# Kernel tuning notes

Measured on AMD Instinct MI355X. Metric: run time of the kernel, lower is better.

## Reference

```python
import jax, jax.numpy as jnp
import numpy as np

TEMP = 1.0

def setup_inputs() -> dict:
    key = jax.random.key(0)
    k1, k2, k3 = jax.random.split(key, 3)
    B, C, H, W = 8, 256, 64, 64
    h = jax.random.normal(k1, (B, C, H, W), dtype=jnp.float32)
    xs = jax.random.normal(k2, (B, C, H, W), dtype=jnp.float32)
    ys = jax.random.normal(k3, (B, C, H, W), dtype=jnp.float32)
    return {"h": h, "xs": xs, "ys": ys}

def reference(h, xs, ys):
    B, C, H, W = h.shape
    Bs, Cs, Hs, Ws = xs.shape
    hf = h.reshape(B, C, H * W)            # [B, C, N]   N = H*W
    xf = xs.reshape(Bs, Cs, Hs * Ws)       # [B, C, M]   M = Hs*Ws
    yf = ys.reshape(ys.shape[0], ys.shape[1], -1)  # [B, C, M]
    # attention[b, n, m] = sum_c h[b,c,n] * xs[b,c,m]
    attn = jnp.einsum('bcn,bcm->bnm', hf, xf)
    attn = jax.nn.softmax(attn / TEMP, axis=2)  # softmax over support positions m
    # xxs[b, c, n] = sum_m ys[b,c,m] * attn[b,n,m]
    xxs = jnp.einsum('bcm,bnm->bcn', yf, attn)
    return xxs.reshape(B, C, H, W)
```

## Files before the change

kernel.cpp:

```cpp
#include <hip/hip_runtime.h>
#include <stdint.h>

#define B_ 8
#define C_ 256
#define N_ 4096
#define M_ 4096
#define NT 64
#define MT 64
#define PP 72
#define L2E 1.44269504f

typedef _Float16 f16x8 __attribute__((ext_vector_type(8)));
typedef _Float16 f16x4 __attribute__((ext_vector_type(4)));
typedef float f32x4 __attribute__((ext_vector_type(4)));

__device__ __forceinline__ void async16(const _Float16* g, _Float16* l) {
    __builtin_amdgcn_global_load_lds(
        (const __attribute__((address_space(1))) void*)g,
        (__attribute__((address_space(3))) void*)l, 16, 0, 0);
}

__global__ __launch_bounds__(256) void kPre(const float* __restrict__ xs,
                                            const float* __restrict__ ys,
                                            _Float16* __restrict__ kt,
                                            _Float16* __restrict__ vb) {
    int bx = blockIdx.x;
    int t = threadIdx.x;
    if (bx < 2048) {
        __shared__ float tile[64][65];
        int b = bx >> 8, rem = bx & 255;
        int c0 = (rem >> 6) * 64, m0 = (rem & 63) * 64;
        int cl = t >> 4, m4 = (t & 15) * 4;
#pragma unroll
        for (int i = 0; i < 4; i++) {
            int c = c0 + cl + i * 16;
            const float4 v = *(const float4*)(xs + ((size_t)(b * C_ + c) * M_) + m0 + m4);
            tile[m4 + 0][cl + i * 16] = v.x;
            tile[m4 + 1][cl + i * 16] = v.y;
            tile[m4 + 2][cl + i * 16] = v.z;
            tile[m4 + 3][cl + i * 16] = v.w;
        }
        __syncthreads();
        int ml = t >> 4, c4 = (t & 15) * 4;
#pragma unroll
        for (int i = 0; i < 4; i++) {
            int m = m0 + ml + i * 16;
            f16x4 o;
            o[0] = (_Float16)tile[ml + i * 16][c4 + 0];
            o[1] = (_Float16)tile[ml + i * 16][c4 + 1];
            o[2] = (_Float16)tile[ml + i * 16][c4 + 2];
            o[3] = (_Float16)tile[ml + i * 16][c4 + 3];
            *(f16x4*)(kt + ((size_t)(b * M_ + m) * C_) + c0 + c4) = o;
        }
    } else {
        size_t i = ((size_t)(bx - 2048) * 256 + t) * 4;
        float4 v = *(const float4*)(ys + i);
        f16x4 o;
        o[0] = (_Float16)v.x; o[1] = (_Float16)v.y;
        o[2] = (_Float16)v.z; o[3] = (_Float16)v.w;
        *(f16x4*)(vb + i) = o;
    }
}

__global__ __launch_bounds__(256, 2) void kAttn(const float* __restrict__ h,
                                                const _Float16* __restrict__ kt,
                                                const _Float16* __restrict__ vb,
                                                float* __restrict__ out) {
    __shared__ _Float16 sK[2][MT * 256];
    __shared__ _Float16 sP[NT * PP];
    __shared__ float sAlpha[NT];
    __shared__ float sL[NT];
    __shared__ int sFlag[2];

    const int t = threadIdx.x;
    const int w = t >> 6, lane = t & 63, quad = lane >> 4, l15 = lane & 15;
    const int b = blockIdx.x >> 6;
    const int n0 = (blockIdx.x & 63) * NT;
    const int nb = w * 16;
    const int cb = w * 64;

    const _Float16* srcKb = kt + (size_t)b * M_ * C_;
    const _Float16* srcVb = vb + (size_t)b * C_ * M_;

    if (t == 0) { sFlag[0] = 0; sFlag[1] = 0; }

    {
        int cl = t >> 4, n4 = (t & 15) * 4;
        for (int i = 0; i < 16; i++) {
            int c = i * 16 + cl;
            const float4 v = *(const float4*)(h + ((size_t)(b * C_ + c) * N_) + n0 + n4);
            float xv[4] = {v.x, v.y, v.z, v.w};
#pragma unroll
            for (int j = 0; j < 4; j++) {
                int row = n4 + j;
                sK[1][row * 256 + (((c >> 3) ^ (row & 31)) << 3) + (c & 7)] = (_Float16)xv[j];
            }
        }
#pragma unroll
        for (int j = 0; j < 8; j++) {
            int row = w * 16 + j * 2 + (lane >> 5);
            int logi = (lane & 31) ^ (row & 31);
            async16(srcKb + (size_t)row * C_ + logi * 8, &sK[0][(w * 16 + j * 2) * 256]);
        }
    }
    __syncthreads();

    f16x8 qf[8];
    {
        int qrow = nb + l15;
#pragma unroll
        for (int ks = 0; ks < 8; ks++)
            qf[ks] = *(const f16x8*)(&sK[1][qrow * 256 + ((((ks << 2) + quad) ^ (qrow & 31)) << 3)]);
    }

    f32x4 o[4][4];
#pragma unroll
    for (int i = 0; i < 4; i++)
#pragma unroll
        for (int j = 0; j < 4; j++)
            o[i][j] = (f32x4){0.f, 0.f, 0.f, 0.f};

    float mst[4], lp[4];
#pragma unroll
    for (int r = 0; r < 4; r++) { mst[r] = -3.0e38f; lp[r] = 0.f; }

    for (int it = 0; it < M_ / MT; it++) {
        const int cur = it & 1, nxt = cur ^ 1;
        const int m0i = it * MT;
        __syncthreads();

        if (t == 0) sFlag[nxt] = 0;

        if (it + 1 < M_ / MT) {
            const _Float16* srcK = srcKb + (size_t)(m0i + MT) * C_;
#pragma unroll
            for (int j = 0; j < 8; j++) {
                int row = w * 16 + j * 2 + (lane >> 5);
                int logi = (lane & 31) ^ (row & 31);
                async16(srcK + (size_t)row * C_ + logi * 8, &sK[nxt][(w * 16 + j * 2) * 256]);
            }
        }

        f16x8 vf[2][4];
#pragma unroll
        for (int ks = 0; ks < 2; ks++)
#pragma unroll
            for (int ct = 0; ct < 4; ct++) {
                int vrow = cb + ct * 16 + l15;
                vf[ks][ct] = *(const f16x8*)(srcVb + (size_t)vrow * M_ + m0i + ks * 32 + quad * 8);
            }

        f32x4 s[4];
#pragma unroll
        for (int mt = 0; mt < 4; mt++) s[mt] = (f32x4){0.f, 0.f, 0.f, 0.f};
#pragma unroll
        for (int ks = 0; ks < 8; ks++) {
#pragma unroll
            for (int mt = 0; mt < 4; mt++) {
                int krow = mt * 16 + l15;
                f16x8 bk = *(const f16x8*)(&sK[cur][krow * 256 + ((((ks << 2) + quad) ^ (krow & 31)) << 3)]);
                s[mt] = __builtin_amdgcn_mfma_f32_16x16x32_f16(qf[ks], bk, s[mt], 0, 0, 0);
            }
        }

#pragma unroll
        for (int r = 0; r < 4; r++) {
            float rowmax = fmaxf(fmaxf(s[0][r], s[1][r]), fmaxf(s[2][r], s[3][r]));
#pragma unroll
            for (int off = 1; off < 16; off <<= 1)
                rowmax = fmaxf(rowmax, __shfl_xor(rowmax, off, 64));
            float al = 1.0f;
            if (rowmax > mst[r]) {
                al = exp2f((mst[r] - rowmax) * L2E);
                mst[r] = rowmax;
            }
            float psum = 0.f;
#pragma unroll
            for (int mt = 0; mt < 4; mt++) {
                float p = exp2f((s[mt][r] - mst[r]) * L2E);
                s[mt][r] = p;
                psum += p;
            }
            lp[r] = lp[r] * al + psum;
            int row = nb + quad * 4 + r;
            if (l15 == 0) {
                sAlpha[row] = al;
                if (al != 1.0f) atomicOr(&sFlag[cur], 1);
            }
#pragma unroll
            for (int mt = 0; mt < 4; mt++)
                sP[row * PP + mt * 16 + l15] = (_Float16)s[mt][r];
        }
        __syncthreads();

        if (sFlag[cur]) {
            float av[4];
#pragma unroll
            for (int nt = 0; nt < 4; nt++) av[nt] = sAlpha[nt * 16 + l15];
#pragma unroll
            for (int ct = 0; ct < 4; ct++)
#pragma unroll
                for (int nt = 0; nt < 4; nt++) {
                    o[ct][nt][0] *= av[nt];
                    o[ct][nt][1] *= av[nt];
                    o[ct][nt][2] *= av[nt];
                    o[ct][nt][3] *= av[nt];
                }
        }

#pragma unroll
        for (int ks = 0; ks < 2; ks++) {
#pragma unroll
            for (int nt = 0; nt < 4; nt++) {
                f16x8 bp = *(const f16x8*)(sP + (nt * 16 + l15) * PP + ks * 32 + quad * 8);
#pragma unroll
                for (int ct = 0; ct < 4; ct++)
                    o[ct][nt] = __builtin_amdgcn_mfma_f32_16x16x32_f16(vf[ks][ct], bp, o[ct][nt], 0, 0, 0);
            }
        }
    }

#pragma unroll
    for (int r = 0; r < 4; r++) {
#pragma unroll
        for (int off = 1; off < 16; off <<= 1)
            lp[r] += __shfl_xor(lp[r], off, 64);
        if (l15 == 0) sL[nb + quad * 4 + r] = lp[r];
    }
    __syncthreads();
    float linv[4];
#pragma unroll
    for (int nt = 0; nt < 4; nt++) linv[nt] = 1.0f / sL[nt * 16 + l15];
#pragma unroll
    for (int ct = 0; ct < 4; ct++)
#pragma unroll
        for (int nt = 0; nt < 4; nt++)
#pragma unroll
            for (int r = 0; r < 4; r++) {
                int c = cb + ct * 16 + quad * 4 + r;
                out[((size_t)(b * C_ + c)) * N_ + n0 + nt * 16 + l15] = o[ct][nt][r] * linv[nt];
            }
}

extern "C" void kernel_launch(void* const* d_in, const int* in_sizes, int n_in,
                              void* d_out, int out_size, void* d_ws, size_t ws_size,
                              hipStream_t stream) {
    const float* h  = (const float*)d_in[0];
    const float* xs = (const float*)d_in[1];
    const float* ys = (const float*)d_in[2];
    float* out = (float*)d_out;

    _Float16* kt  = (_Float16*)d_ws;
    _Float16* vbb = kt + (size_t)B_ * M_ * C_;

    kPre<<<dim3(2048 + 8192), 256, 0, stream>>>(xs, ys, kt, vbb);
    kAttn<<<dim3(B_ * (N_ / NT)), 256, 0, stream>>>(h, kt, vbb, out);
}
```

Baseline: 359.6 us.

## Transpose QK MFMA, simplify softmax reductions, replace syncthreads with tuned waitcnt barriers

Swaps the MFMA operand order for S so each lane holds one query row's scores. Row max and sum then need only two cross-quad shuffles instead of four per row, and P can be stored as packed f16x4 writes. Full __syncthreads are replaced by explicit s_waitcnt plus s_barrier, and V global loads are hoisted ahead of the K async prefetch behind a sched_barrier. The MFMA sections are wrapped in s_setprio to favour matrix issue. The manual waitcnt placement risks stalls or races if the counter semantics for global_load_lds are misjudged, for example vmcnt(0) at the loop top also waits on the V loads.

```diff
diff --git a/kernel.cpp b/kernel.cpp
--- a/kernel.cpp
+++ b/kernel.cpp
@@ -103,7 +103,8 @@
             async16(srcKb + (size_t)row * C_ + logi * 8, &sK[0][(w * 16 + j * 2) * 256]);
         }
     }
-    __syncthreads();
+    asm volatile("s_waitcnt lgkmcnt(0)" ::: "memory");
+    __builtin_amdgcn_s_barrier();
 
     f16x8 qf[8];
     {
@@ -112,6 +113,7 @@
         for (int ks = 0; ks < 8; ks++)
             qf[ks] = *(const f16x8*)(&sK[1][qrow * 256 + ((((ks << 2) + quad) ^ (qrow & 31)) << 3)]);
     }
+    asm volatile("s_waitcnt lgkmcnt(0)" ::: "memory");
 
     f32x4 o[4][4];
 #pragma unroll
@@ -120,16 +122,25 @@
         for (int j = 0; j < 4; j++)
             o[i][j] = (f32x4){0.f, 0.f, 0.f, 0.f};
 
-    float mst[4], lp[4];
-#pragma unroll
-    for (int r = 0; r < 4; r++) { mst[r] = -3.0e38f; lp[r] = 0.f; }
+    float mst = -3.0e38f, lp = 0.f;
 
     for (int it = 0; it < M_ / MT; it++) {
         const int cur = it & 1, nxt = cur ^ 1;
         const int m0i = it * MT;
-        __syncthreads();
+        asm volatile("s_waitcnt vmcnt(0)" ::: "memory");
+        __builtin_amdgcn_s_barrier();
 
         if (t == 0) sFlag[nxt] = 0;
+
+        f16x8 vf[2][4];
+#pragma unroll
+        for (int ks = 0; ks < 2; ks++)
+#pragma unroll
+            for (int ct = 0; ct < 4; ct++) {
+                int vrow = cb + ct * 16 + l15;
+                vf[ks][ct] = *(const f16x8*)(srcVb + (size_t)vrow * M_ + m0i + ks * 32 + quad * 8);
+            }
+        __builtin_amdgcn_sched_barrier(0);
 
         if (it + 1 < M_ / MT) {
             const _Float16* srcK = srcKb + (size_t)(m0i + MT) * C_;
@@ -141,57 +152,59 @@
             }
         }
 
-        f16x8 vf[2][4];
-#pragma unroll
-        for (int ks = 0; ks < 2; ks++)
-#pragma unroll
-            for (int ct = 0; ct < 4; ct++) {
-                int vrow = cb + ct * 16 + l15;
-                vf[ks][ct] = *(const f16x8*)(srcVb + (size_t)vrow * M_ + m0i + ks * 32 + quad * 8);
-            }
-
         f32x4 s[4];
 #pragma unroll
         for (int mt = 0; mt < 4; mt++) s[mt] = (f32x4){0.f, 0.f, 0.f, 0.f};
+        __builtin_amdgcn_s_setprio(1);
 #pragma unroll
         for (int ks = 0; ks < 8; ks++) {
 #pragma unroll
             for (int mt = 0; mt < 4; mt++) {
                 int krow = mt * 16 + l15;
                 f16x8 bk = *(const f16x8*)(&sK[cur][krow * 256 + ((((ks << 2) + quad) ^ (krow & 31)) << 3)]);
-                s[mt] = __builtin_amdgcn_mfma_f32_16x16x32_f16(qf[ks], bk, s[mt], 0, 0, 0);
-            }
-        }
-
-#pragma unroll
-        for (int r = 0; r < 4; r++) {
-            float rowmax = fmaxf(fmaxf(s[0][r], s[1][r]), fmaxf(s[2][r], s[3][r]));
-#pragma unroll
-            for (int off = 1; off < 16; off <<= 1)
-                rowmax = fmaxf(rowmax, __shfl_xor(rowmax, off, 64));
-            float al = 1.0f;
-            if (rowmax > mst[r]) {
-                al = exp2f((mst[r] - rowmax) * L2E);
-                mst[r] = rowmax;
-            }
-            float psum = 0.f;
-#pragma unroll
-            for (int mt = 0; mt < 4; mt++) {
-                float p = exp2f((s[mt][r] - mst[r]) * L2E);
+                s[mt] = __builtin_amdgcn_mfma_f32_16x16x32_f16(bk, qf[ks], s[mt], 0, 0, 0);
+            }
+        }
+        __builtin_amdgcn_s_setprio(0);
+
+        float rowmax = fmaxf(fmaxf(fmaxf(s[0][0], s[0][1]), fmaxf(s[0][2], s[0][3])),
+                             fmaxf(fmaxf(s[1][0], s[1][1]), fmaxf(s[1][2], s[1][3])));
+        rowmax = fmaxf(rowmax, fmaxf(fmaxf(fmaxf(s[2][0], s[2][1]), fmaxf(s[2][2], s[2][3])),
+                                     fmaxf(fmaxf(s[3][0], s[3][1]), fmaxf(s[3][2], s[3][3]))));
+        rowmax = fmaxf(rowmax, __shfl_xor(rowmax, 16, 64));
+        rowmax = fmaxf(rowmax, __shfl_xor(rowmax, 32, 64));
+        float al = 1.0f;
+        if (rowmax > mst) {
+            al = exp2f((mst - rowmax) * L2E);
+            mst = rowmax;
+        }
+        const float mb = mst * L2E;
+        float psum = 0.f;
+#pragma unroll
+        for (int mt = 0; mt < 4; mt++)
+#pragma unroll
+            for (int r = 0; r < 4; r++) {
+                float p = exp2f(s[mt][r] * L2E - mb);
                 s[mt][r] = p;
                 psum += p;
             }
-            lp[r] = lp[r] * al + psum;
-            int row = nb + quad * 4 + r;
-            if (l15 == 0) {
-                sAlpha[row] = al;
-                if (al != 1.0f) atomicOr(&sFlag[cur], 1);
-            }
-#pragma unroll
-            for (int mt = 0; mt < 4; mt++)
-                sP[row * PP + mt * 16 + l15] = (_Float16)s[mt][r];
-        }
-        __syncthreads();
+        lp = lp * al + psum;
+        if (quad == 0) {
+            sAlpha[nb + l15] = al;
+            if (al != 1.0f) atomicOr(&sFlag[cur], 1);
+        }
+#pragma unroll
+        for (int mt = 0; mt < 4; mt++) {
+            f16x4 pk;
+            pk[0] = (_Float16)s[mt][0];
+            pk[1] = (_Float16)s[mt][1];
+            pk[2] = (_Float16)s[mt][2];
+            pk[3] = (_Float16)s[mt][3];
+            *(f16x4*)(&sP[(nb + l15) * PP + mt * 16 + quad * 4]) = pk;
+        }
+
+        asm volatile("s_waitcnt lgkmcnt(0)" ::: "memory");
+        __builtin_amdgcn_s_barrier();
 
         if (sFlag[cur]) {
             float av[4];
@@ -208,6 +221,7 @@
                 }
         }
 
+        __builtin_amdgcn_s_setprio(1);
 #pragma unroll
         for (int ks = 0; ks < 2; ks++) {
 #pragma unroll
@@ -218,15 +232,12 @@
                     o[ct][nt] = __builtin_amdgcn_mfma_f32_16x16x32_f16(vf[ks][ct], bp, o[ct][nt], 0, 0, 0);
             }
         }
-    }
-
-#pragma unroll
-    for (int r = 0; r < 4; r++) {
-#pragma unroll
-        for (int off = 1; off < 16; off <<= 1)
-            lp[r] += __shfl_xor(lp[r], off, 64);
-        if (l15 == 0) sL[nb + quad * 4 + r] = lp[r];
-    }
+        __builtin_amdgcn_s_setprio(0);
+    }
+
+    lp += __shfl_xor(lp, 16, 64);
+    lp += __shfl_xor(lp, 32, 64);
+    if (quad == 0) sL[nb + l15] = lp;
     __syncthreads();
     float linv[4];
 #pragma unroll
```

After: 361.2 us. About the same (+0.5%).
